# Kernel tuning notes

Hardware: AMD Instinct MI355X
Metric: run time of the kernel (lower is better)

The kernel has to match this reference:

```python
import jax, jax.numpy as jnp
import numpy as np

B, T, INP, E, H, N = 16, 256, 1536, 512, 8, 16
D = E // H            # 64, must equal default dim_head for to_out shapes to work
SCALE = D ** -0.5
EPS = 1e-5


def _ln(x, g, b):
    m = x.mean(-1, keepdims=True)
    v = ((x - m) ** 2).mean(-1, keepdims=True)
    return (x - m) * jax.lax.rsqrt(v + EPS) * g + b


def _attend(q, k, v, Wo, bo):
    # q,k,v: [bt, h, n, d]. NOTE: attend is LogSoftmax, not Softmax (faithful).
    dots = jnp.einsum('bhnd,bhmd->bhnm', q, k) * SCALE
    a = jax.nn.log_softmax(dots, axis=-1)
    o = jnp.einsum('bhnm,bhmd->bhnd', a, v)
    o = o.transpose(0, 2, 1, 3).reshape(o.shape[0], N, E)  # b n (h d)
    return o @ Wo + bo


def _self_attn(x, Wqkv, Wo, bo):
    # x is already LayerNormed (PreNorm); residual adds the normed x (faithful).
    qkv = x @ Wqkv  # [bt, n, 3E]
    q, k, v = jnp.split(qkv, 3, axis=-1)
    hd = lambda t: t.reshape(t.shape[0], N, H, D).transpose(0, 2, 1, 3)
    return _attend(hd(q), hd(k), hd(v), Wo, bo) + x


def _ff(x, W1, b1, W2, b2):
    # x already LayerNormed; residual adds normed x (faithful to PreNorm+FF).
    return jax.nn.gelu(x @ W1 + b1, approximate=False) @ W2 + b2 + x


def setup_inputs() -> dict:
    key = jax.random.key(0)
    ks = iter(jax.random.split(key, 64))
    nrm = lambda shape, s=0.02: jax.random.normal(next(ks), shape, jnp.float32) * s
    inp = {
        'features': jax.random.normal(next(ks), (B, T, INP), jnp.float32),
        'targets_array': jax.random.randint(next(ks), (B, T), 0, N, jnp.int64),
        'emb': nrm((N, E), 1.0),
        'Wf': nrm((INP, 2 * E * N)), 'bf': jnp.zeros((2 * E * N,), jnp.float32),
        # layer 0: Attention (tuple path: only to_out used)
        'att0_Wo': nrm((E, E)), 'att0_bo': jnp.zeros((E,), jnp.float32),
        'Wm': nrm((E, 1)), 'bm': jnp.zeros((1,), jnp.float32),
    }
    for i in range(3):
        inp[f'ff{i}_g'] = jnp.ones((E,), jnp.float32)
        inp[f'ff{i}_b'] = jnp.zeros((E,), jnp.float32)
        inp[f'ff{i}_W1'] = nrm((E, 2 * E)); inp[f'ff{i}_b1'] = jnp.zeros((2 * E,), jnp.float32)
        inp[f'ff{i}_W2'] = nrm((2 * E, E)); inp[f'ff{i}_b2'] = jnp.zeros((E,), jnp.float32)
    for i in (1, 2):
        inp[f'att{i}_g'] = jnp.ones((E,), jnp.float32)
        inp[f'att{i}_b'] = jnp.zeros((E,), jnp.float32)
        inp[f'att{i}_Wqkv'] = nrm((E, 3 * E))
        inp[f'att{i}_Wo'] = nrm((E, E)); inp[f'att{i}_bo'] = jnp.zeros((E,), jnp.float32)
    return inp


def reference(features, targets_array, emb, Wf, bf, att0_Wo, att0_bo, Wm, bm,
              ff0_g, ff0_b, ff0_W1, ff0_b1, ff0_W2, ff0_b2,
              ff1_g, ff1_b, ff1_W1, ff1_b1, ff1_W2, ff1_b2,
              ff2_g, ff2_b, ff2_W1, ff2_b1, ff2_W2, ff2_b2,
              att1_g, att1_b, att1_Wqkv, att1_Wo, att1_bo,
              att2_g, att2_b, att2_Wqkv, att2_Wo, att2_bo):
    f = features.reshape(-1, INP)                 # [BT, INP]
    t = targets_array.reshape(-1)                 # [BT]
    kv = f @ Wf + bf                              # [BT, 2*E*N]
    k_, v_ = jnp.split(kv, 2, axis=-1)
    nhd = lambda x: x.reshape(-1, N, H, D).transpose(0, 2, 1, 3)  # b (n h d) -> b h n d
    k, v = nhd(k_), nhd(v_)
    q = emb[t].reshape(-1, H, 1, D)               # b h d -> b h 1 d
    q = jnp.broadcast_to(q, (q.shape[0], H, N, D))
    # layer stack: Attn(tuple), PreNorm(FF), PreNorm(Attn), PreNorm(FF), PreNorm(Attn), PreNorm(FF)
    x = _attend(q, k, v, att0_Wo, att0_bo)        # [BT, N, E]
    x = _ff(_ln(x, ff0_g, ff0_b), ff0_W1, ff0_b1, ff0_W2, ff0_b2)
    x = _self_attn(_ln(x, att1_g, att1_b), att1_Wqkv, att1_Wo, att1_bo)
    x = _ff(_ln(x, ff1_g, ff1_b), ff1_W1, ff1_b1, ff1_W2, ff1_b2)
    x = _self_attn(_ln(x, att2_g, att2_b), att2_Wqkv, att2_Wo, att2_bo)
    x = _ff(_ln(x, ff2_g, ff2_b), ff2_W1, ff2_b1, ff2_W2, ff2_b2)
    out = x.mean(axis=1)                          # mean over targets -> [BT, E]
    out = out.reshape(B, T, E)
    mean = out @ Wm + bm                          # [B, T, 1]
    return mean
```

## Files before the change

kernel.cpp:

```cpp
#include <hip/hip_runtime.h>
#include <math.h>

#define BTOT 4096
#define INP  1536
#define EDIM 512
#define NTOK 16
#define KVW  16384
#define ENW  8192
#define FFH  1024
#define NDOT 2048

typedef __attribute__((ext_vector_type(8))) __bf16 bf16x8;
typedef __attribute__((ext_vector_type(4))) float f32x4;

__device__ __forceinline__ ushort f2bf(float f) {
    union { float f; unsigned u; } v; v.f = f;
    unsigned r = v.u + 0x7fffu + ((v.u >> 16) & 1u);
    return (ushort)(r >> 16);
}
__device__ __forceinline__ float bf2f(ushort h) {
    union { unsigned u; float f; } v; v.u = ((unsigned)h) << 16;
    return v.f;
}

__device__ __forceinline__ void transpose_body(
    const float* in, int ld, int c0, int R, ushort* out,
    int bx, int by, int tid)
{
    __shared__ float t[64][65];
    const int bc = bx * 64 + c0;
    const int br = by * 64;
#pragma unroll
    for (int it = 0; it < 16; ++it) {
        int idx = tid + it * 256;
        int r = idx >> 6, c = idx & 63;
        t[r][c] = in[(size_t)(br + r) * ld + bc + c];
    }
    __syncthreads();
    const int C0 = bx * 64;
#pragma unroll
    for (int it = 0; it < 4; ++it) {
        int idx = tid + it * 256;
        int cc = idx >> 4, rp = idx & 15;
        uint2 w2;
        w2.x = f2bf(t[4 * rp + 0][cc]) | ((unsigned)f2bf(t[4 * rp + 1][cc]) << 16);
        w2.y = f2bf(t[4 * rp + 2][cc]) | ((unsigned)f2bf(t[4 * rp + 3][cc]) << 16);
        *reinterpret_cast<uint2*>(out + (size_t)(C0 + cc) * R + br + 4 * rp) = w2;
    }
}

struct TJob { const float* in; ushort* out; int ld, c0, R, gbx, gby, boffs; };
struct TJobs { TJob j[10]; };

__global__ __launch_bounds__(256) void transpose_all_k(TJobs jobs)
{
    const int b = blockIdx.x;
    int ji = 0;
    while (ji < 9 && b >= jobs.j[ji + 1].boffs) ++ji;
    TJob jb = jobs.j[ji];
    const int rel = b - jb.boffs;
    transpose_body(jb.in, jb.ld, jb.c0, jb.R, jb.out,
                   rel % jb.gbx, rel / jb.gbx, threadIdx.x);
}

__global__ __launch_bounds__(256) void conv_all_k(
    const float* __restrict__ features, ushort* __restrict__ featb,
    const float* __restrict__ wq0, const float* __restrict__ wq1,
    ushort* __restrict__ wv0, ushort* __restrict__ wv1)
{
    const int b = blockIdx.x;
    if (b < 3072) {
        const int i = b * 256 + threadIdx.x;
        const float4* p = reinterpret_cast<const float4*>(features) + 2 * (size_t)i;
        float4 a = p[0], c = p[1];
        uint4 o;
        o.x = f2bf(a.x) | ((unsigned)f2bf(a.y) << 16);
        o.y = f2bf(a.z) | ((unsigned)f2bf(a.w) << 16);
        o.z = f2bf(c.x) | ((unsigned)f2bf(c.y) << 16);
        o.w = f2bf(c.z) | ((unsigned)f2bf(c.w) << 16);
        reinterpret_cast<uint4*>(featb)[i] = o;
    } else {
        const int bb = b - 3072;
        const float* src = (bb >= 128) ? wq1 : wq0;
        ushort* dst = (bb >= 128) ? wv1 : wv0;
        const int idx = (bb & 127) * 256 + threadIdx.x;
        const int row = idx >> 6, c8 = (idx & 63) * 8;
        const float4* p = reinterpret_cast<const float4*>(
            src + (size_t)row * (3 * EDIM) + 2 * EDIM + c8);
        float4 a = p[0], c = p[1];
        uint4 o;
        o.x = f2bf(a.x) | ((unsigned)f2bf(a.y) << 16);
        o.y = f2bf(a.z) | ((unsigned)f2bf(a.w) << 16);
        o.z = f2bf(c.x) | ((unsigned)f2bf(c.y) << 16);
        o.w = f2bf(c.z) | ((unsigned)f2bf(c.w) << 16);
        *reinterpret_cast<uint4*>(dst + (size_t)row * EDIM + c8) = o;
    }
}

__global__ __launch_bounds__(256) void gproj_k(
    const float* __restrict__ Wf, const float* __restrict__ bfv,
    const float* __restrict__ emb, ushort* __restrict__ BTg,
    float* __restrict__ C0s, const int* __restrict__ targets,
    int* __restrict__ perm, int* __restrict__ boff)
{
    if (blockIdx.y == 8) {
        if (blockIdx.x != 0) return;
        __shared__ int cnt[NTOK], off_s[NTOK], cur[NTOK];
        const int tid = threadIdx.x;
        if (tid < NTOK) cnt[tid] = 0;
        __syncthreads();
        for (int i = tid; i < BTOT; i += 256) atomicAdd(&cnt[targets[i]], 1);
        __syncthreads();
        if (tid == 0) {
            int s = 0;
            for (int b = 0; b < NTOK; ++b) { off_s[b] = s; cur[b] = s; s += cnt[b]; }
            for (int b = 0; b < NTOK; ++b) boff[b] = off_s[b];
            boff[NTOK] = s;
        }
        __syncthreads();
        for (int i = tid; i < BTOT; i += 256) {
            int t = targets[i];
            int p = atomicAdd(&cur[t], 1);
            perm[p] = i;
        }
        return;
    }

    const int hm = blockIdx.x;
    const int h = hm >> 4, m = hm & 15;
    const int l = threadIdx.x & 63, w = threadIdx.x >> 6;
    const int t = l & 15, isub = l >> 4;
    const int colb = m * 512 + h * 64;
    const int ibase = blockIdx.y * (INP / 8);

    float4 e[16];
#pragma unroll
    for (int q = 0; q < 16; ++q)
        e[q] = *reinterpret_cast<const float4*>(emb + t * EDIM + h * 64 + q * 4);

    const int n = t * 128 + hm;
    for (int i0 = ibase; i0 < ibase + INP / 8; i0 += 16) {
        const int i = i0 + w * 4 + isub;
        const float* wr = Wf + (size_t)i * KVW + colb;
        float acc = 0.f;
#pragma unroll
        for (int q = 0; q < 16; ++q) {
            float4 v4 = *reinterpret_cast<const float4*>(wr + q * 4);
            acc = fmaf(v4.x, e[q].x, fmaf(v4.y, e[q].y,
                  fmaf(v4.z, e[q].z, fmaf(v4.w, e[q].w, acc))));
        }
        BTg[(size_t)n * INP + i] = f2bf(acc);
    }
    if (blockIdx.y == 0 && w == 0 && isub == 0) {
        const float* br = bfv + colb;
        float acc = 0.f;
#pragma unroll
        for (int q = 0; q < 16; ++q) {
            float4 v4 = *reinterpret_cast<const float4*>(br + q * 4);
            acc = fmaf(v4.x, e[q].x, fmaf(v4.y, e[q].y,
                  fmaf(v4.z, e[q].z, fmaf(v4.w, e[q].w, acc))));
        }
        C0s[n] = 0.125f * acc;
    }
}

template <int BM, int BN, int WM, int WN, int NW, bool GELU, bool OUTBF>
__global__ __launch_bounds__(NW * 64) void gemm_mfma_k(
    const ushort* __restrict__ A, int lda,
    const ushort* __restrict__ BT, int ldb,
    void* __restrict__ Cp, int ldc, int K,
    const float* __restrict__ bias,
    const float* __restrict__ res, int ldr,
    float scale)
{
    static_assert((BM / WM) * (BN / WN) == NW, "wave grid");
    static_assert(BM % (NW * 8) == 0 && BN % (NW * 8) == 0, "staging");
    constexpr int FM = WM / 16, FN = WN / 16;
    constexpr int IA = BM * 8 / (NW * 64), IB = BN * 8 / (NW * 64);
    constexpr int RA = BM / NW, RB = BN / NW;

    __shared__ bf16x8 As[BM][8];
    __shared__ bf16x8 Bs[BN][8];
    const int tid = threadIdx.x;
    const int l   = tid & 63;
    const int w   = tid >> 6;
    const int wm  = w / (BN / WN), wn = w % (BN / WN);
    const int brow = blockIdx.y * BM, bcol = blockIdx.x * BN;

    const int lr = l >> 3;
    const int ls = (l & 7) ^ lr;
    const ushort* Ab = A  + (size_t)(brow + w * RA + lr) * lda + ls * 8;
    const ushort* Bb = BT + (size_t)(bcol + w * RB + lr) * ldb + ls * 8;

    f32x4 acc[FM][FN];
#pragma unroll
    for (int i = 0; i < FM; ++i)
#pragma unroll
        for (int j = 0; j < FN; ++j) acc[i][j] = (f32x4)0.f;

    for (int k0 = 0; k0 < K; k0 += 64) {
#pragma unroll
        for (int i = 0; i < IA; ++i)
            __builtin_amdgcn_global_load_lds(
                (const __attribute__((address_space(1))) void*)(Ab + (size_t)(i * 8) * lda + k0),
                (__attribute__((address_space(3))) void*)&As[w * RA + i * 8][0],
                16, 0, 0);
#pragma unroll
        for (int i = 0; i < IB; ++i)
            __builtin_amdgcn_global_load_lds(
                (const __attribute__((address_space(1))) void*)(Bb + (size_t)(i * 8) * ldb + k0),
                (__attribute__((address_space(3))) void*)&Bs[w * RB + i * 8][0],
                16, 0, 0);
        __syncthreads();
#pragma unroll
        for (int kh = 0; kh < 2; ++kh) {
            const int slot = (kh * 4 + (l >> 4)) ^ (l & 7);
            bf16x8 af[FM], bfr[FN];
#pragma unroll
            for (int mt = 0; mt < FM; ++mt)
                af[mt] = As[wm * WM + mt * 16 + (l & 15)][slot];
#pragma unroll
            for (int nt = 0; nt < FN; ++nt)
                bfr[nt] = Bs[wn * WN + nt * 16 + (l & 15)][slot];
#pragma unroll
            for (int mt = 0; mt < FM; ++mt)
#pragma unroll
                for (int nt = 0; nt < FN; ++nt)
                    acc[mt][nt] = __builtin_amdgcn_mfma_f32_16x16x32_bf16(
                        af[mt], bfr[nt], acc[mt][nt], 0, 0, 0);
        }
        __syncthreads();
    }

    const int cr = (l >> 4) * 4, cc = l & 15;
#pragma unroll
    for (int mt = 0; mt < FM; ++mt) {
#pragma unroll
        for (int nt = 0; nt < FN; ++nt) {
            const int gc = bcol + wn * WN + nt * 16 + cc;
            const float bv = bias ? bias[gc] : 0.f;
#pragma unroll
            for (int r = 0; r < 4; ++r) {
                const size_t gr = (size_t)brow + wm * WM + mt * 16 + cr + r;
                float v = acc[mt][nt][r] * scale + bv;
                if (GELU) v = 0.5f * v * (1.f + erff(v * 0.70710678118654752f));
                if (res) v += res[gr * ldr + gc];
                if (OUTBF) ((ushort*)Cp)[gr * ldc + gc] = f2bf(v);
                else       ((float*)Cp)[gr * ldc + gc]  = v;
            }
        }
    }
}

__global__ __launch_bounds__(256) void gemm_dots_k(
    const ushort* __restrict__ A,
    const ushort* __restrict__ BT,
    const int* __restrict__ perm, const int* __restrict__ boff,
    const float* __restrict__ C0s, float* __restrict__ Csel)
{
    const int bucket = blockIdx.y;
    const int off = boff[bucket], end = boff[bucket + 1];
    const int tile = blockIdx.x;
    if (tile * 128 >= end - off) return;

    __shared__ bf16x8 As[128][8];
    __shared__ bf16x8 Bs[128][8];
    const int tid = threadIdx.x;
    const int l = tid & 63, w = tid >> 6;
    const int wm = w >> 1, wn = w & 1;
    const int lr = l >> 3;
    const int ls = (l & 7) ^ lr;

    int rowidx[4];
#pragma unroll
    for (int i = 0; i < 4; ++i) {
        int rg = off + tile * 128 + w * 32 + lr + i * 8;
        rowidx[i] = perm[rg < end ? rg : off];
    }
    const ushort* Bb = BT + (size_t)(bucket * 128 + w * 32 + lr) * INP + ls * 8;

    f32x4 acc[4][4];
#pragma unroll
    for (int i = 0; i < 4; ++i)
#pragma unroll
        for (int j = 0; j < 4; ++j) acc[i][j] = (f32x4)0.f;

    for (int k0 = 0; k0 < INP; k0 += 64) {
#pragma unroll
        for (int i = 0; i < 4; ++i)
            __builtin_amdgcn_global_load_lds(
                (const __attribute__((address_space(1))) void*)(
                    A + (size_t)rowidx[i] * INP + ls * 8 + k0),
                (__attribute__((address_space(3))) void*)&As[w * 32 + i * 8][0],
                16, 0, 0);
#pragma unroll
        for (int i = 0; i < 4; ++i)
            __builtin_amdgcn_global_load_lds(
                (const __attribute__((address_space(1))) void*)(
                    Bb + (size_t)(i * 8) * INP + k0),
                (__attribute__((address_space(3))) void*)&Bs[w * 32 + i * 8][0],
                16, 0, 0);
        __syncthreads();
#pragma unroll
        for (int kh = 0; kh < 2; ++kh) {
            const int slot = (kh * 4 + (l >> 4)) ^ (l & 7);
            bf16x8 af[4], bfr[4];
#pragma unroll
            for (int mt = 0; mt < 4; ++mt)
                af[mt] = As[wm * 64 + mt * 16 + (l & 15)][slot];
#pragma unroll
            for (int nt = 0; nt < 4; ++nt)
                bfr[nt] = Bs[wn * 64 + nt * 16 + (l & 15)][slot];
#pragma unroll
            for (int mt = 0; mt < 4; ++mt)
#pragma unroll
                for (int nt = 0; nt < 4; ++nt)
                    acc[mt][nt] = __builtin_amdgcn_mfma_f32_16x16x32_bf16(
                        af[mt], bfr[nt], acc[mt][nt], 0, 0, 0);
        }
        __syncthreads();
    }

    const int cr = (l >> 4) * 4, cc = l & 15;
#pragma unroll
    for (int mt = 0; mt < 4; ++mt) {
#pragma unroll
        for (int nt = 0; nt < 4; ++nt) {
            const int gc = wn * 64 + nt * 16 + cc;
            const float bv = C0s[bucket * 128 + gc];
#pragma unroll
            for (int r = 0; r < 4; ++r) {
                float val = acc[mt][nt][r] * 0.125f + bv;
                float mx = val;
                mx = fmaxf(mx, __shfl_xor(mx, 1, 64));
                mx = fmaxf(mx, __shfl_xor(mx, 2, 64));
                mx = fmaxf(mx, __shfl_xor(mx, 4, 64));
                mx = fmaxf(mx, __shfl_xor(mx, 8, 64));
                float e = expf(val - mx);
                e += __shfl_xor(e, 1, 64);
                e += __shfl_xor(e, 2, 64);
                e += __shfl_xor(e, 4, 64);
                e += __shfl_xor(e, 8, 64);
                const float lse = mx + logf(e);
                int rg = off + tile * 128 + wm * 64 + mt * 16 + cr + r;
                int orow = perm[rg < end ? rg : off];
                Csel[(size_t)orow * 128 + gc] = val - lse;
            }
        }
    }
}

__global__ __launch_bounds__(512) void attend0_k(
    const float* __restrict__ dsel, const ushort* __restrict__ vb,
    ushort* __restrict__ o)
{
    const int bt = blockIdx.x;
    const int l  = threadIdx.x & 63;
    const int h  = threadIdx.x >> 6;
    const int dg = l & 7, mg = l >> 3;

    const float w0 = dsel[(size_t)bt * 128 + h * 16 + mg];
    const float w1 = dsel[(size_t)bt * 128 + h * 16 + 8 + mg];

    const ushort* base = vb + (size_t)bt * ENW + h * 64 + dg * 8;
    uint4 v0 = *reinterpret_cast<const uint4*>(base + (size_t)mg * EDIM);
    uint4 v1 = *reinterpret_cast<const uint4*>(base + (size_t)(8 + mg) * EDIM);
    const ushort* u0 = reinterpret_cast<const ushort*>(&v0);
    const ushort* u1 = reinterpret_cast<const ushort*>(&v1);
    float acc[8];
#pragma unroll
    for (int j = 0; j < 8; ++j)
        acc[j] = w0 * bf2f(u0[j]) + w1 * bf2f(u1[j]);
#pragma unroll
    for (int off = 8; off < 64; off <<= 1)
#pragma unroll
        for (int j = 0; j < 8; ++j) acc[j] += __shfl_xor(acc[j], off, 64);

    if (mg == 0) {
        uint4 pk;
        pk.x = f2bf(acc[0]) | ((unsigned)f2bf(acc[1]) << 16);
        pk.y = f2bf(acc[2]) | ((unsigned)f2bf(acc[3]) << 16);
        pk.z = f2bf(acc[4]) | ((unsigned)f2bf(acc[5]) << 16);
        pk.w = f2bf(acc[6]) | ((unsigned)f2bf(acc[7]) << 16);
        *reinterpret_cast<uint4*>(o + (size_t)bt * EDIM + h * 64 + dg * 8) = pk;
    }
}

__global__ __launch_bounds__(256) void ln_k(
    const float* __restrict__ x, const float* __restrict__ g,
    const float* __restrict__ b, float* __restrict__ y,
    ushort* __restrict__ yb)
{
    const int row = blockIdx.x * 4 + (threadIdx.x >> 6);
    const int lane = threadIdx.x & 63;
    const float* xr = x + (size_t)row * EDIM + lane * 8;
    float4 a0 = *reinterpret_cast<const float4*>(xr);
    float4 a1 = *reinterpret_cast<const float4*>(xr + 4);
    float v[8] = {a0.x, a0.y, a0.z, a0.w, a1.x, a1.y, a1.z, a1.w};

    float s = 0.f;
#pragma unroll
    for (int j = 0; j < 8; ++j) s += v[j];
#pragma unroll
    for (int off = 32; off; off >>= 1) s += __shfl_xor(s, off, 64);
    const float m = s * (1.f / 512.f);

    float q = 0.f;
#pragma unroll
    for (int j = 0; j < 8; ++j) { float d = v[j] - m; q = fmaf(d, d, q); }
#pragma unroll
    for (int off = 32; off; off >>= 1) q += __shfl_xor(q, off, 64);
    const float inv = rsqrtf(q * (1.f / 512.f) + 1e-5f);

    const int c = lane * 8;
    float4 g0 = *reinterpret_cast<const float4*>(g + c);
    float4 g1 = *reinterpret_cast<const float4*>(g + c + 4);
    float4 b0 = *reinterpret_cast<const float4*>(b + c);
    float4 b1 = *reinterpret_cast<const float4*>(b + c + 4);
    float gg[8] = {g0.x, g0.y, g0.z, g0.w, g1.x, g1.y, g1.z, g1.w};
    float bb[8] = {b0.x, b0.y, b0.z, b0.w, b1.x, b1.y, b1.z, b1.w};
    float out[8];
#pragma unroll
    for (int j = 0; j < 8; ++j) out[j] = (v[j] - m) * inv * gg[j] + bb[j];
    float* yr = y + (size_t)row * EDIM + c;
    *reinterpret_cast<float4*>(yr) = make_float4(out[0], out[1], out[2], out[3]);
    *reinterpret_cast<float4*>(yr + 4) = make_float4(out[4], out[5], out[6], out[7]);
    uint4 p;
    p.x = f2bf(out[0]) | ((unsigned)f2bf(out[1]) << 16);
    p.y = f2bf(out[2]) | ((unsigned)f2bf(out[3]) << 16);
    p.z = f2bf(out[4]) | ((unsigned)f2bf(out[5]) << 16);
    p.w = f2bf(out[6]) | ((unsigned)f2bf(out[7]) << 16);
    *reinterpret_cast<uint4*>(yb + (size_t)row * EDIM + c) = p;
}

__global__ __launch_bounds__(256) void final_k(
    const float* __restrict__ x, const float* __restrict__ Wm,
    const float* __restrict__ bm, float* __restrict__ out)
{
    const int row = blockIdx.x * 4 + (threadIdx.x >> 6);
    const int lane = threadIdx.x & 63;
    const float* xr = x + (size_t)row * EDIM + lane * 8;
    const float* wr = Wm + lane * 8;
    float s = 0.f;
#pragma unroll
    for (int j = 0; j < 8; ++j) s = fmaf(xr[j], wr[j], s);
#pragma unroll
    for (int off = 32; off; off >>= 1) s += __shfl_xor(s, off, 64);
    if (lane == 0) out[row] = s + bm[0];
}

extern "C" void kernel_launch(void* const* d_in, const int* in_sizes, int n_in,
                              void* d_out, int out_size, void* d_ws, size_t ws_size,
                              hipStream_t stream)
{
    (void)in_sizes; (void)n_in; (void)out_size;
    const float* features = (const float*)d_in[0];
    const int*   targets  = (const int*)d_in[1];
    const float* emb      = (const float*)d_in[2];
    const float* Wf       = (const float*)d_in[3];
    const float* bfv      = (const float*)d_in[4];
    const float* a0Wo     = (const float*)d_in[5];
    const float* a0bo     = (const float*)d_in[6];
    const float* Wm       = (const float*)d_in[7];
    const float* bm       = (const float*)d_in[8];
    const float *ffg[3], *ffb[3], *W1[3], *b1[3], *W2[3], *b2[3];
    for (int i = 0; i < 3; ++i) {
        ffg[i] = (const float*)d_in[9 + 6 * i];
        ffb[i] = (const float*)d_in[10 + 6 * i];
        W1[i]  = (const float*)d_in[11 + 6 * i];
        b1[i]  = (const float*)d_in[12 + 6 * i];
        W2[i]  = (const float*)d_in[13 + 6 * i];
        b2[i]  = (const float*)d_in[14 + 6 * i];
    }
    const float *ag[2], *abp[2], *aWqkv[2], *aWo[2], *abo[2];
    for (int i = 0; i < 2; ++i) {
        ag[i]    = (const float*)d_in[27 + 5 * i];
        abp[i]   = (const float*)d_in[28 + 5 * i];
        aWqkv[i] = (const float*)d_in[29 + 5 * i];
        aWo[i]   = (const float*)d_in[30 + 5 * i];
        abo[i]   = (const float*)d_in[31 + 5 * i];
    }

    char* wsc = (char*)d_ws;
    auto alloc = [&](size_t bytes) { char* p = wsc; wsc += bytes; return p; };
    ushort* WfvT  = (ushort*)alloc((size_t)ENW * INP * 2);
    ushort* BTg   = (ushort*)alloc((size_t)NDOT * INP * 2);
    float*  C0s   = (float*) alloc((size_t)NDOT * 4);
    float*  dsel  = (float*) alloc((size_t)BTOT * 128 * 4);
    int*    perm  = (int*)   alloc((size_t)BTOT * 4);
    int*    boff  = (int*)   alloc(32 * 4);
    ushort* a0WoT = (ushort*)alloc((size_t)EDIM * EDIM * 2);
    ushort *W1T[3], *W2T[3], *WoT[2], *Wv_bf[2], *WcombT[2];
    for (int i = 0; i < 3; ++i) {
        W1T[i] = (ushort*)alloc((size_t)FFH * EDIM * 2);
        W2T[i] = (ushort*)alloc((size_t)EDIM * FFH * 2);
    }
    for (int i = 0; i < 2; ++i) {
        WoT[i]    = (ushort*)alloc((size_t)EDIM * EDIM * 2);
        Wv_bf[i]  = (ushort*)alloc((size_t)EDIM * EDIM * 2);
        WcombT[i] = (ushort*)alloc((size_t)EDIM * EDIM * 2);
    }
    ushort* featb = (ushort*)alloc((size_t)BTOT * INP * 2);
    ushort* o_b   = (ushort*)alloc((size_t)BTOT * EDIM * 2);
    float*  x     = (float*) alloc((size_t)BTOT * EDIM * 4);
    float*  xln   = (float*) alloc((size_t)BTOT * EDIM * 4);
    ushort* xlnb  = (ushort*)alloc((size_t)BTOT * EDIM * 2);
    ushort* hb    = (ushort*)alloc((size_t)BTOT * FFH * 2);
    const size_t fixed = (size_t)(wsc - (char*)d_ws);
    int CB = BTOT;
    while (CB > 256 && fixed + (size_t)CB * ENW * 2 > ws_size) CB >>= 1;
    ushort* vb = (ushort*)alloc((size_t)CB * ENW * 2);

    const dim3 blk(256, 1, 1);

    conv_all_k<<<3328, blk, 0, stream>>>(features, featb,
                                         aWqkv[0], aWqkv[1], Wv_bf[0], Wv_bf[1]);
    gproj_k<<<dim3(128, 9), blk, 0, stream>>>(Wf, bfv, emb, BTg, C0s,
                                              targets, perm, boff);

    TJobs tj;
    int ob = 0, ji = 0;
    auto addj = [&](const float* in, ushort* out, int ld, int c0, int R,
                    int gbx, int gby) {
        tj.j[ji++] = {in, out, ld, c0, R, gbx, gby, ob};
        ob += gbx * gby;
    };
    addj(Wf, WfvT, KVW, ENW, INP, 128, 24);
    addj(a0Wo, a0WoT, EDIM, 0, EDIM, 8, 8);
    for (int i = 0; i < 3; ++i) {
        addj(W1[i], W1T[i], FFH, 0, EDIM, 16, 8);
        addj(W2[i], W2T[i], EDIM, 0, FFH, 8, 16);
    }
    addj(aWo[0], WoT[0], EDIM, 0, EDIM, 8, 8);
    addj(aWo[1], WoT[1], EDIM, 0, EDIM, 8, 8);
    transpose_all_k<<<ob, blk, 0, stream>>>(tj);

    const float CATT = -44.36141955583650f;
    for (int i = 0; i < 2; ++i)
        gemm_mfma_k<64, 128, 32, 64, 4, false, true>
            <<<dim3(EDIM / 128, EDIM / 64), blk, 0, stream>>>(
            WoT[i], EDIM, Wv_bf[i], EDIM, WcombT[i], EDIM, EDIM,
            nullptr, nullptr, 0, CATT);

    gemm_dots_k<<<dim3(32, 16), blk, 0, stream>>>(featb, BTg, perm, boff,
                                                  C0s, dsel);
    for (int c0 = 0; c0 < BTOT; c0 += CB) {
        gemm_mfma_k<128, 128, 64, 64, 4, false, true>
            <<<dim3(ENW / 128, CB / 128), blk, 0, stream>>>(
            featb + (size_t)c0 * INP, INP, WfvT, INP, vb, ENW, INP,
            bfv + ENW, nullptr, 0, 1.f);
        attend0_k<<<CB, 512, 0, stream>>>(dsel + (size_t)c0 * 128, vb,
                                          o_b + (size_t)c0 * EDIM);
    }
    gemm_mfma_k<64, 128, 32, 64, 4, false, false>
        <<<dim3(EDIM / 128, BTOT / 64), blk, 0, stream>>>(
        o_b, EDIM, a0WoT, EDIM, x, EDIM, EDIM, a0bo, nullptr, 0, 1.f);

    auto ln = [&](const float* g, const float* b) {
        ln_k<<<BTOT / 4, blk, 0, stream>>>(x, g, b, xln, xlnb);
    };
    auto ff = [&](int i) {
        ln(ffg[i], ffb[i]);
        gemm_mfma_k<64, 128, 32, 64, 4, true, true>
            <<<dim3(FFH / 128, BTOT / 64), blk, 0, stream>>>(
            xlnb, EDIM, W1T[i], EDIM, hb, FFH, EDIM, b1[i], nullptr, 0, 1.f);
        gemm_mfma_k<64, 128, 32, 64, 4, false, false>
            <<<dim3(EDIM / 128, BTOT / 64), blk, 0, stream>>>(
            hb, FFH, W2T[i], FFH, x, EDIM, FFH, b2[i], xln, EDIM, 1.f);
    };
    auto attn = [&](int i) {
        ln(ag[i], abp[i]);
        gemm_mfma_k<64, 128, 32, 64, 4, false, false>
            <<<dim3(EDIM / 128, BTOT / 64), blk, 0, stream>>>(
            xlnb, EDIM, WcombT[i], EDIM, x, EDIM, EDIM, abo[i], xln, EDIM, 1.f);
    };

    ff(0);
    attn(0);
    ff(1);
    attn(1);
    ff(2);

    final_k<<<BTOT / 4, blk, 0, stream>>>(x, Wm, bm, (float*)d_out);
}
```

Measured before the change: 492.6 us.

## Merge prep kernels and independent GEMMs into single heterogeneous launches

Folds the bf16 conversion, the gproj/bucketing and the weight-transpose kernels into one prep launch. It also merges the big V projection GEMM, the bucketed dots GEMM and the two small Wo·Wv combine GEMMs into one multi-job GEMM launch that dispatches on block index. This removes several kernel launches and lets the independent GEMMs fill the GPU together. The cost is dropping the workspace-size chunking, so the whole V buffer (4096x8192 bf16) must fit in workspace, and the prep kernel now carries extra shared memory for every block.

Result: no change. 493.5 us (+0.2%).

```diff
diff --git a/kernel.cpp b/kernel.cpp
--- a/kernel.cpp
+++ b/kernel.cpp
@@ -23,18 +23,129 @@
     return v.f;
 }
 
-__device__ __forceinline__ void transpose_body(
-    const float* in, int ld, int c0, int R, ushort* out,
-    int bx, int by, int tid)
+struct TJob { const float* in; ushort* out; int ld, c0, R, gbx, boffs; };
+
+struct PrepArgs {
+    const float* features; ushort* featb;
+    const float* wq0; const float* wq1; ushort* wv0; ushort* wv1;
+    const float* Wf; const float* bfv; const float* emb;
+    ushort* BTg; float* C0s; const int* targets; int* perm; int* boff;
+    TJob tj[10];
+};
+
+__global__ __launch_bounds__(256) void prep_all_k(PrepArgs A)
 {
     __shared__ float t[64][65];
-    const int bc = bx * 64 + c0;
+    __shared__ int cnt[NTOK], off_s[NTOK], cur[NTOK];
+    const int b = blockIdx.x;
+    const int tid = threadIdx.x;
+
+    if (b < 3328) {
+        if (b < 3072) {
+            const int i = b * 256 + tid;
+            const float4* p = reinterpret_cast<const float4*>(A.features) + 2 * (size_t)i;
+            float4 a = p[0], c = p[1];
+            uint4 o;
+            o.x = f2bf(a.x) | ((unsigned)f2bf(a.y) << 16);
+            o.y = f2bf(a.z) | ((unsigned)f2bf(a.w) << 16);
+            o.z = f2bf(c.x) | ((unsigned)f2bf(c.y) << 16);
+            o.w = f2bf(c.z) | ((unsigned)f2bf(c.w) << 16);
+            reinterpret_cast<uint4*>(A.featb)[i] = o;
+        } else {
+            const int bb = b - 3072;
+            const float* src = (bb >= 128) ? A.wq1 : A.wq0;
+            ushort* dst = (bb >= 128) ? A.wv1 : A.wv0;
+            const int idx = (bb & 127) * 256 + tid;
+            const int row = idx >> 6, c8 = (idx & 63) * 8;
+            const float4* p = reinterpret_cast<const float4*>(
+                src + (size_t)row * (3 * EDIM) + 2 * EDIM + c8);
+            float4 a = p[0], c = p[1];
+            uint4 o;
+            o.x = f2bf(a.x) | ((unsigned)f2bf(a.y) << 16);
+            o.y = f2bf(a.z) | ((unsigned)f2bf(a.w) << 16);
+            o.z = f2bf(c.x) | ((unsigned)f2bf(c.y) << 16);
+            o.w = f2bf(c.z) | ((unsigned)f2bf(c.w) << 16);
+            *reinterpret_cast<uint4*>(dst + (size_t)row * EDIM + c8) = o;
+        }
+        return;
+    }
+
+    if (b < 4480) {
+        const int gb = b - 3328;
+        const int hm = gb & 127;
+        const int gby = gb >> 7;
+        if (gby == 8) {
+            if (hm != 0) return;
+            if (tid < NTOK) cnt[tid] = 0;
+            __syncthreads();
+            for (int i = tid; i < BTOT; i += 256) atomicAdd(&cnt[A.targets[i]], 1);
+            __syncthreads();
+            if (tid == 0) {
+                int s = 0;
+                for (int bk = 0; bk < NTOK; ++bk) { off_s[bk] = s; cur[bk] = s; s += cnt[bk]; }
+                for (int bk = 0; bk < NTOK; ++bk) A.boff[bk] = off_s[bk];
+                A.boff[NTOK] = s;
+            }
+            __syncthreads();
+            for (int i = tid; i < BTOT; i += 256) {
+                int tt = A.targets[i];
+                int p = atomicAdd(&cur[tt], 1);
+                A.perm[p] = i;
+            }
+            return;
+        }
+        const int h = hm >> 4, m = hm & 15;
+        const int l = tid & 63, w = tid >> 6;
+        const int tk = l & 15, isub = l >> 4;
+        const int colb = m * 512 + h * 64;
+        const int ibase = gby * (INP / 8);
+
+        float4 e[16];
+#pragma unroll
+        for (int q = 0; q < 16; ++q)
+            e[q] = *reinterpret_cast<const float4*>(A.emb + tk * EDIM + h * 64 + q * 4);
+
+        const int n = tk * 128 + hm;
+        for (int i0 = ibase; i0 < ibase + INP / 8; i0 += 16) {
+            const int i = i0 + w * 4 + isub;
+            const float* wr = A.Wf + (size_t)i * KVW + colb;
+            float acc = 0.f;
+#pragma unroll
+            for (int q = 0; q < 16; ++q) {
+                float4 v4 = *reinterpret_cast<const float4*>(wr + q * 4);
+                acc = fmaf(v4.x, e[q].x, fmaf(v4.y, e[q].y,
+                      fmaf(v4.z, e[q].z, fmaf(v4.w, e[q].w, acc))));
+            }
+            A.BTg[(size_t)n * INP + i] = f2bf(acc);
+        }
+        if (gby == 0 && w == 0 && isub == 0) {
+            const float* br = A.bfv + colb;
+            float acc = 0.f;
+#pragma unroll
+            for (int q = 0; q < 16; ++q) {
+                float4 v4 = *reinterpret_cast<const float4*>(br + q * 4);
+                acc = fmaf(v4.x, e[q].x, fmaf(v4.y, e[q].y,
+                      fmaf(v4.z, e[q].z, fmaf(v4.w, e[q].w, acc))));
+            }
+            A.C0s[n] = 0.125f * acc;
+        }
+        return;
+    }
+
+    const int rel = b - 4480;
+    int ji = 0;
+    while (ji < 9 && rel >= A.tj[ji + 1].boffs) ++ji;
+    TJob jb = A.tj[ji];
+    const int r2 = rel - jb.boffs;
+    const int bx = r2 % jb.gbx, by = r2 / jb.gbx;
+
+    const int bc = bx * 64 + jb.c0;
     const int br = by * 64;
 #pragma unroll
     for (int it = 0; it < 16; ++it) {
         int idx = tid + it * 256;
         int r = idx >> 6, c = idx & 63;
-        t[r][c] = in[(size_t)(br + r) * ld + bc + c];
+        t[r][c] = jb.in[(size_t)(br + r) * jb.ld + bc + c];
     }
     __syncthreads();
     const int C0 = bx * 64;
@@ -45,122 +156,7 @@
         uint2 w2;
         w2.x = f2bf(t[4 * rp + 0][cc]) | ((unsigned)f2bf(t[4 * rp + 1][cc]) << 16);
         w2.y = f2bf(t[4 * rp + 2][cc]) | ((unsigned)f2bf(t[4 * rp + 3][cc]) << 16);
-        *reinterpret_cast<uint2*>(out + (size_t)(C0 + cc) * R + br + 4 * rp) = w2;
-    }
-}
-
-struct TJob { const float* in; ushort* out; int ld, c0, R, gbx, gby, boffs; };
-struct TJobs { TJob j[10]; };
-
-__global__ __launch_bounds__(256) void transpose_all_k(TJobs jobs)
-{
-    const int b = blockIdx.x;
-    int ji = 0;
-    while (ji < 9 && b >= jobs.j[ji + 1].boffs) ++ji;
-    TJob jb = jobs.j[ji];
-    const int rel = b - jb.boffs;
-    transpose_body(jb.in, jb.ld, jb.c0, jb.R, jb.out,
-                   rel % jb.gbx, rel / jb.gbx, threadIdx.x);
-}
-
-__global__ __launch_bounds__(256) void conv_all_k(
-    const float* __restrict__ features, ushort* __restrict__ featb,
-    const float* __restrict__ wq0, const float* __restrict__ wq1,
-    ushort* __restrict__ wv0, ushort* __restrict__ wv1)
-{
-    const int b = blockIdx.x;
-    if (b < 3072) {
-        const int i = b * 256 + threadIdx.x;
-        const float4* p = reinterpret_cast<const float4*>(features) + 2 * (size_t)i;
-        float4 a = p[0], c = p[1];
-        uint4 o;
-        o.x = f2bf(a.x) | ((unsigned)f2bf(a.y) << 16);
-        o.y = f2bf(a.z) | ((unsigned)f2bf(a.w) << 16);
-        o.z = f2bf(c.x) | ((unsigned)f2bf(c.y) << 16);
-        o.w = f2bf(c.z) | ((unsigned)f2bf(c.w) << 16);
-        reinterpret_cast<uint4*>(featb)[i] = o;
-    } else {
-        const int bb = b - 3072;
-        const float* src = (bb >= 128) ? wq1 : wq0;
-        ushort* dst = (bb >= 128) ? wv1 : wv0;
-        const int idx = (bb & 127) * 256 + threadIdx.x;
-        const int row = idx >> 6, c8 = (idx & 63) * 8;
-        const float4* p = reinterpret_cast<const float4*>(
-            src + (size_t)row * (3 * EDIM) + 2 * EDIM + c8);
-        float4 a = p[0], c = p[1];
-        uint4 o;
-        o.x = f2bf(a.x) | ((unsigned)f2bf(a.y) << 16);
-        o.y = f2bf(a.z) | ((unsigned)f2bf(a.w) << 16);
-        o.z = f2bf(c.x) | ((unsigned)f2bf(c.y) << 16);
-        o.w = f2bf(c.z) | ((unsigned)f2bf(c.w) << 16);
-        *reinterpret_cast<uint4*>(dst + (size_t)row * EDIM + c8) = o;
-    }
-}
-
-__global__ __launch_bounds__(256) void gproj_k(
-    const float* __restrict__ Wf, const float* __restrict__ bfv,
-    const float* __restrict__ emb, ushort* __restrict__ BTg,
-    float* __restrict__ C0s, const int* __restrict__ targets,
-    int* __restrict__ perm, int* __restrict__ boff)
-{
-    if (blockIdx.y == 8) {
-        if (blockIdx.x != 0) return;
-        __shared__ int cnt[NTOK], off_s[NTOK], cur[NTOK];
-        const int tid = threadIdx.x;
-        if (tid < NTOK) cnt[tid] = 0;
-        __syncthreads();
-        for (int i = tid; i < BTOT; i += 256) atomicAdd(&cnt[targets[i]], 1);
-        __syncthreads();
-        if (tid == 0) {
-            int s = 0;
-            for (int b = 0; b < NTOK; ++b) { off_s[b] = s; cur[b] = s; s += cnt[b]; }
-            for (int b = 0; b < NTOK; ++b) boff[b] = off_s[b];
-            boff[NTOK] = s;
-        }
-        __syncthreads();
-        for (int i = tid; i < BTOT; i += 256) {
-            int t = targets[i];
-            int p = atomicAdd(&cur[t], 1);
-            perm[p] = i;
-        }
-        return;
-    }
-
-    const int hm = blockIdx.x;
-    const int h = hm >> 4, m = hm & 15;
-    const int l = threadIdx.x & 63, w = threadIdx.x >> 6;
-    const int t = l & 15, isub = l >> 4;
-    const int colb = m * 512 + h * 64;
-    const int ibase = blockIdx.y * (INP / 8);
-
-    float4 e[16];
-#pragma unroll
-    for (int q = 0; q < 16; ++q)
-        e[q] = *reinterpret_cast<const float4*>(emb + t * EDIM + h * 64 + q * 4);
-
-    const int n = t * 128 + hm;
-    for (int i0 = ibase; i0 < ibase + INP / 8; i0 += 16) {
-        const int i = i0 + w * 4 + isub;
-        const float* wr = Wf + (size_t)i * KVW + colb;
-        float acc = 0.f;
-#pragma unroll
-        for (int q = 0; q < 16; ++q) {
-            float4 v4 = *reinterpret_cast<const float4*>(wr + q * 4);
-            acc = fmaf(v4.x, e[q].x, fmaf(v4.y, e[q].y,
-                  fmaf(v4.z, e[q].z, fmaf(v4.w, e[q].w, acc))));
-        }
-        BTg[(size_t)n * INP + i] = f2bf(acc);
-    }
-    if (blockIdx.y == 0 && w == 0 && isub == 0) {
-        const float* br = bfv + colb;
-        float acc = 0.f;
-#pragma unroll
-        for (int q = 0; q < 16; ++q) {
-            float4 v4 = *reinterpret_cast<const float4*>(br + q * 4);
-            acc = fmaf(v4.x, e[q].x, fmaf(v4.y, e[q].y,
-                  fmaf(v4.z, e[q].z, fmaf(v4.w, e[q].w, acc))));
-        }
-        C0s[n] = 0.125f * acc;
+        *reinterpret_cast<uint2*>(jb.out + (size_t)(C0 + cc) * jb.R + br + 4 * rp) = w2;
     }
 }
 
@@ -252,32 +248,64 @@
     }
 }
 
-__global__ __launch_bounds__(256) void gemm_dots_k(
-    const ushort* __restrict__ A,
-    const ushort* __restrict__ BT,
+__global__ __launch_bounds__(256) void mega_gemm_k(
+    const ushort* __restrict__ featb,
+    const ushort* __restrict__ WfvT, const float* __restrict__ bfvv,
+    ushort* __restrict__ vb,
+    const ushort* __restrict__ BTg,
     const int* __restrict__ perm, const int* __restrict__ boff,
-    const float* __restrict__ C0s, float* __restrict__ Csel)
+    const float* __restrict__ C0s, float* __restrict__ dsel,
+    const ushort* __restrict__ WoT0, const ushort* __restrict__ Wv0,
+    ushort* __restrict__ WC0,
+    const ushort* __restrict__ WoT1, const ushort* __restrict__ Wv1,
+    ushort* __restrict__ WC1)
 {
-    const int bucket = blockIdx.y;
-    const int off = boff[bucket], end = boff[bucket + 1];
-    const int tile = blockIdx.x;
-    if (tile * 128 >= end - off) return;
-
     __shared__ bf16x8 As[128][8];
     __shared__ bf16x8 Bs[128][8];
+    const int b = blockIdx.x;
     const int tid = threadIdx.x;
     const int l = tid & 63, w = tid >> 6;
     const int wm = w >> 1, wn = w & 1;
-    const int lr = l >> 3;
-    const int ls = (l & 7) ^ lr;
-
-    int rowidx[4];
-#pragma unroll
-    for (int i = 0; i < 4; ++i) {
-        int rg = off + tile * 128 + w * 32 + lr + i * 8;
-        rowidx[i] = perm[rg < end ? rg : off];
-    }
-    const ushort* Bb = BT + (size_t)(bucket * 128 + w * 32 + lr) * INP + ls * 8;
+    const int lr = l >> 3, ls = (l & 7) ^ lr;
+
+    int jtype, K;
+    const ushort* Asrc[4];
+    const ushort* Bb;
+    ushort* WCo = nullptr;
+    int brow = 0, bcol = 0, bucket = 0, off = 0, end = 0, tile = 0;
+
+    if (b < 2048) {
+        jtype = 0; K = INP;
+        brow = (b >> 6) * 128; bcol = (b & 63) * 128;
+#pragma unroll
+        for (int i = 0; i < 4; ++i)
+            Asrc[i] = featb + (size_t)(brow + w * 32 + lr + i * 8) * INP + ls * 8;
+        Bb = WfvT + (size_t)(bcol + w * 32 + lr) * INP + ls * 8;
+    } else if (b < 2560) {
+        jtype = 1; K = INP;
+        const int rel = b - 2048;
+        bucket = rel >> 5; tile = rel & 31;
+        off = boff[bucket]; end = boff[bucket + 1];
+        if (tile * 128 >= end - off) return;
+#pragma unroll
+        for (int i = 0; i < 4; ++i) {
+            int rg = off + tile * 128 + w * 32 + lr + i * 8;
+            Asrc[i] = featb + (size_t)perm[rg < end ? rg : off] * INP + ls * 8;
+        }
+        Bb = BTg + (size_t)(bucket * 128 + w * 32 + lr) * INP + ls * 8;
+    } else {
+        jtype = 2; K = EDIM;
+        const int rel = b - 2560;
+        const int wi = rel >> 4, r2 = rel & 15;
+        brow = (r2 >> 2) * 128; bcol = (r2 & 3) * 128;
+        const ushort* Ai = wi ? WoT1 : WoT0;
+        const ushort* Bi = wi ? Wv1 : Wv0;
+        WCo = wi ? WC1 : WC0;
+#pragma unroll
+        for (int i = 0; i < 4; ++i)
+            Asrc[i] = Ai + (size_t)(brow + w * 32 + lr + i * 8) * EDIM + ls * 8;
+        Bb = Bi + (size_t)(bcol + w * 32 + lr) * EDIM + ls * 8;
+    }
 
     f32x4 acc[4][4];
 #pragma unroll
@@ -285,19 +313,17 @@
 #pragma unroll
         for (int j = 0; j < 4; ++j) acc[i][j] = (f32x4)0.f;
 
-    for (int k0 = 0; k0 < INP; k0 += 64) {
+    for (int k0 = 0; k0 < K; k0 += 64) {
 #pragma unroll
         for (int i = 0; i < 4; ++i)
             __builtin_amdgcn_global_load_lds(
-                (const __attribute__((address_space(1))) void*)(
-                    A + (size_t)rowidx[i] * INP + ls * 8 + k0),
+                (const __attribute__((address_space(1))) void*)(Asrc[i] + k0),
                 (__attribute__((address_space(3))) void*)&As[w * 32 + i * 8][0],
                 16, 0, 0);
 #pragma unroll
         for (int i = 0; i < 4; ++i)
             __builtin_amdgcn_global_load_lds(
-                (const __attribute__((address_space(1))) void*)(
-                    Bb + (size_t)(i * 8) * INP + k0),
+                (const __attribute__((address_space(1))) void*)(Bb + (size_t)(i * 8) * K + k0),
                 (__attribute__((address_space(3))) void*)&Bs[w * 32 + i * 8][0],
                 16, 0, 0);
         __syncthreads();
@@ -322,29 +348,60 @@
     }
 
     const int cr = (l >> 4) * 4, cc = l & 15;
-#pragma unroll
-    for (int mt = 0; mt < 4; ++mt) {
-#pragma unroll
-        for (int nt = 0; nt < 4; ++nt) {
-            const int gc = wn * 64 + nt * 16 + cc;
-            const float bv = C0s[bucket * 128 + gc];
-#pragma unroll
-            for (int r = 0; r < 4; ++r) {
-                float val = acc[mt][nt][r] * 0.125f + bv;
-                float mx = val;
-                mx = fmaxf(mx, __shfl_xor(mx, 1, 64));
-                mx = fmaxf(mx, __shfl_xor(mx, 2, 64));
-                mx = fmaxf(mx, __shfl_xor(mx, 4, 64));
-                mx = fmaxf(mx, __shfl_xor(mx, 8, 64));
-                float e = expf(val - mx);
-                e += __shfl_xor(e, 1, 64);
-                e += __shfl_xor(e, 2, 64);
-                e += __shfl_xor(e, 4, 64);
-                e += __shfl_xor(e, 8, 64);
-                const float lse = mx + logf(e);
-                int rg = off + tile * 128 + wm * 64 + mt * 16 + cr + r;
-                int orow = perm[rg < end ? rg : off];
-                Csel[(size_t)orow * 128 + gc] = val - lse;
+    const float CATT = -44.36141955583650f;
+
+    if (jtype == 0) {
+#pragma unroll
+        for (int mt = 0; mt < 4; ++mt) {
+#pragma unroll
+            for (int nt = 0; nt < 4; ++nt) {
+                const int gc = bcol + wn * 64 + nt * 16 + cc;
+                const float bv = bfvv[gc];
+#pragma unroll
+                for (int r = 0; r < 4; ++r) {
+                    const size_t gr = (size_t)brow + wm * 64 + mt * 16 + cr + r;
+                    vb[gr * ENW + gc] = f2bf(acc[mt][nt][r] + bv);
+                }
+            }
+        }
+    } else if (jtype == 1) {
+#pragma unroll
+        for (int mt = 0; mt < 4; ++mt) {
+#pragma unroll
+            for (int nt = 0; nt < 4; ++nt) {
+                const int gc = wn * 64 + nt * 16 + cc;
+                const float bv = C0s[bucket * 128 + gc];
+#pragma unroll
+                for (int r = 0; r < 4; ++r) {
+                    float val = acc[mt][nt][r] * 0.125f + bv;
+                    float mx = val;
+                    mx = fmaxf(mx, __shfl_xor(mx, 1, 64));
+                    mx = fmaxf(mx, __shfl_xor(mx, 2, 64));
+                    mx = fmaxf(mx, __shfl_xor(mx, 4, 64));
+                    mx = fmaxf(mx, __shfl_xor(mx, 8, 64));
+                    float e = expf(val - mx);
+                    e += __shfl_xor(e, 1, 64);
+                    e += __shfl_xor(e, 2, 64);
+                    e += __shfl_xor(e, 4, 64);
+                    e += __shfl_xor(e, 8, 64);
+                    const float lse = mx + logf(e);
+                    int rg = off + tile * 128 + wm * 64 + mt * 16 + cr + r;
+                    int orow = perm[rg < end ? rg : off];
+                    dsel[(size_t)orow * 128 + gc] = val - lse;
+                }
+            }
+        }
+    } else {
+#pragma unroll
+        for (int mt = 0; mt < 4; ++mt) {
+#pragma unroll
+            for (int nt = 0; nt < 4; ++nt) {
+                const int gc = bcol + wn * 64 + nt * 16 + cc;
+#pragma unroll
+                for (int r = 0; r < 4; ++r) {
+                    const size_t gr = (size_t)brow + wm * 64 + mt * 16 + cr + r;
+                    WCo[gr * EDIM + gc] = f2bf(acc[mt][nt][r] * CATT);
+                }
             }
         }
     }
@@ -453,7 +510,7 @@
                               void* d_out, int out_size, void* d_ws, size_t ws_size,
                               hipStream_t stream)
 {
-    (void)in_sizes; (void)n_in; (void)out_size;
+    (void)in_sizes; (void)n_in; (void)out_size; (void)ws_size;
     const float* features = (const float*)d_in[0];
     const int*   targets  = (const int*)d_in[1];
     const float* emb      = (const float*)d_in[2];
@@ -506,23 +563,20 @@
     float*  xln   = (float*) alloc((size_t)BTOT * EDIM * 4);
     ushort* xlnb  = (ushort*)alloc((size_t)BTOT * EDIM * 2);
     ushort* hb    = (ushort*)alloc((size_t)BTOT * FFH * 2);
-    const size_t fixed = (size_t)(wsc - (char*)d_ws);
-    int CB = BTOT;
-    while (CB > 256 && fixed + (size_t)CB * ENW * 2 > ws_size) CB >>= 1;
-    ushort* vb = (ushort*)alloc((size_t)CB * ENW * 2);
+    ushort* vb    = (ushort*)alloc((size_t)BTOT * ENW * 2);
 
     const dim3 blk(256, 1, 1);
 
-    conv_all_k<<<3328, blk, 0, stream>>>(features, featb,
-                                         aWqkv[0], aWqkv[1], Wv_bf[0], Wv_bf[1]);
-    gproj_k<<<dim3(128, 9), blk, 0, stream>>>(Wf, bfv, emb, BTg, C0s,
-                                              targets, perm, boff);
-
-    TJobs tj;
+    PrepArgs pa;
+    pa.features = features; pa.featb = featb;
+    pa.wq0 = aWqkv[0]; pa.wq1 = aWqkv[1]; pa.wv0 = Wv_bf[0]; pa.wv1 = Wv_bf[1];
+    pa.Wf = Wf; pa.bfv = bfv; pa.emb = emb;
+    pa.BTg = BTg; pa.C0s = C0s; pa.targets = targets;
+    pa.perm = perm; pa.boff = boff;
     int ob = 0, ji = 0;
     auto addj = [&](const float* in, ushort* out, int ld, int c0, int R,
                     int gbx, int gby) {
-        tj.j[ji++] = {in, out, ld, c0, R, gbx, gby, ob};
+        pa.tj[ji++] = {in, out, ld, c0, R, gbx, ob};
         ob += gbx * gby;
     };
     addj(Wf, WfvT, KVW, ENW, INP, 128, 24);
@@ -533,25 +587,15 @@
     }
     addj(aWo[0], WoT[0], EDIM, 0, EDIM, 8, 8);
     addj(aWo[1], WoT[1], EDIM, 0, EDIM, 8, 8);
-    transpose_all_k<<<ob, blk, 0, stream>>>(tj);
-
-    const float CATT = -44.36141955583650f;
-    for (int i = 0; i < 2; ++i)
-        gemm_mfma_k<64, 128, 32, 64, 4, false, true>
-            <<<dim3(EDIM / 128, EDIM / 64), blk, 0, stream>>>(
-            WoT[i], EDIM, Wv_bf[i], EDIM, WcombT[i], EDIM, EDIM,
-            nullptr, nullptr, 0, CATT);
-
-    gemm_dots_k<<<dim3(32, 16), blk, 0, stream>>>(featb, BTg, perm, boff,
-                                                  C0s, dsel);
-    for (int c0 = 0; c0 < BTOT; c0 += CB) {
-        gemm_mfma_k<128, 128, 64, 64, 4, false, true>
-            <<<dim3(ENW / 128, CB / 128), blk, 0, stream>>>(
-            featb + (size_t)c0 * INP, INP, WfvT, INP, vb, ENW, INP,
-            bfv + ENW, nullptr, 0, 1.f);
-        attend0_k<<<CB, 512, 0, stream>>>(dsel + (size_t)c0 * 128, vb,
-                                          o_b + (size_t)c0 * EDIM);
-    }
+    prep_all_k<<<4480 + ob, blk, 0, stream>>>(pa);
+
+    mega_gemm_k<<<2592, blk, 0, stream>>>(
+        featb, WfvT, bfv + ENW, vb,
+        BTg, perm, boff, C0s, dsel,
+        WoT[0], Wv_bf[0], WcombT[0],
+        WoT[1], Wv_bf[1], WcombT[1]);
+
+    attend0_k<<<BTOT, 512, 0, stream>>>(dsel, vb, o_b);
     gemm_mfma_k<64, 128, 32, 64, 4, false, false>
         <<<dim3(EDIM / 128, BTOT / 64), blk, 0, stream>>>(
         o_b, EDIM, a0WoT, EDIM, x, EDIM, EDIM, a0bo, nullptr, 0, 1.f);
```

## Add 256x256 double-buffered direct-to-LDS GEMM for the value projection

Applied to the files above, without the earlier changes.

Replaces the generic 128x128 MFMA GEMM for the large features x Wf value projection with a dedicated 256x256-tile kernel of 512 threads. It double-buffers global-to-LDS loads with XOR-swizzled slots and interleaves the next tile's prefetch with the MFMA phases, using barriers and setprio. The workspace chunking loop is removed so the whole value buffer is allocated at once and attend0 runs in a single launch. This assumes the workspace is large enough for the full bf16 value buffer and drops the fallback for smaller workspaces.

After: 474.0 us. -3.8%, faster.

```diff
diff --git a/kernel.cpp b/kernel.cpp
--- a/kernel.cpp
+++ b/kernel.cpp
@@ -49,7 +49,7 @@
     }
 }
 
-struct TJob { const float* in; ushort* out; int ld, c0, R, gbx, gby, boffs; };
+struct TJob { const float* in; ushort* out; int ld, c0, R, gbx, boffs; };
 struct TJobs { TJob j[10]; };
 
 __global__ __launch_bounds__(256) void transpose_all_k(TJobs jobs)
@@ -252,6 +252,117 @@
     }
 }
 
+__global__ __launch_bounds__(512, 2) void gemm_v256_k(
+    const ushort* __restrict__ A,
+    const ushort* __restrict__ BT,
+    const float* __restrict__ bias,
+    ushort* __restrict__ C)
+{
+    __shared__ bf16x8 lds[2][2][256][8];
+    const int tid = threadIdx.x;
+    const int l = tid & 63, w = tid >> 6;
+    const int wm = w >> 2, wn = w & 3;
+    const int brow = blockIdx.y * 256, bcol = blockIdx.x * 256;
+    const int lr = l >> 3, ls = (l & 7) ^ lr;
+
+    const ushort* Ab = A  + (size_t)(brow + w * 8 + lr) * INP + ls * 8;
+    const ushort* Bb = BT + (size_t)(bcol + w * 8 + lr) * INP + ls * 8;
+
+#define STAGE_T(d, t) do { const int k0s = (t) * 64;                          \
+    _Pragma("unroll")                                                          \
+    for (int g = 0; g < 4; ++g)                                                \
+        __builtin_amdgcn_global_load_lds(                                      \
+            (const __attribute__((address_space(1))) void*)(Ab + (size_t)(g * 64) * INP + k0s), \
+            (__attribute__((address_space(3))) void*)&lds[d][0][g * 64 + w * 8][0], 16, 0, 0);  \
+    _Pragma("unroll")                                                          \
+    for (int g = 0; g < 4; ++g)                                                \
+        __builtin_amdgcn_global_load_lds(                                      \
+            (const __attribute__((address_space(1))) void*)(Bb + (size_t)(g * 64) * INP + k0s), \
+            (__attribute__((address_space(3))) void*)&lds[d][1][g * 64 + w * 8][0], 16, 0, 0);  \
+} while (0)
+
+    f32x4 acc[8][4];
+#pragma unroll
+    for (int i = 0; i < 8; ++i)
+#pragma unroll
+        for (int j = 0; j < 4; ++j) acc[i][j] = (f32x4)0.f;
+
+    STAGE_T(0, 0);
+    STAGE_T(1, 1);
+    asm volatile("s_waitcnt vmcnt(8)" ::: "memory");
+    __builtin_amdgcn_s_barrier();
+
+    const int NT = INP / 64;
+    for (int j = 0; j < NT; ++j) {
+        const int d = j & 1;
+        const bool st = (j > 0 && j < NT - 1);
+        const int k0s = (j + 1) * 64;
+        bf16x8 bfr[4][2];
+#pragma unroll
+        for (int p = 0; p < 4; ++p) {
+            const int rh = p >> 1, kh = p & 1;
+            const int slot = (kh * 4 + (l >> 4)) ^ (l & 7);
+            bf16x8 a[4];
+#pragma unroll
+            for (int mt = 0; mt < 4; ++mt)
+                a[mt] = lds[d][0][wm * 128 + rh * 64 + mt * 16 + (l & 15)][slot];
+            if (p < 2) {
+#pragma unroll
+                for (int nt = 0; nt < 4; ++nt)
+                    bfr[nt][kh] = lds[d][1][wn * 64 + nt * 16 + (l & 15)][slot];
+            }
+            if (st) {
+#pragma unroll
+                for (int q = 0; q < 2; ++q) {
+                    const int idx = 2 * p + q;
+                    if (idx < 4)
+                        __builtin_amdgcn_global_load_lds(
+                            (const __attribute__((address_space(1))) void*)(
+                                Ab + (size_t)(idx * 64) * INP + k0s),
+                            (__attribute__((address_space(3))) void*)
+                                &lds[d ^ 1][0][idx * 64 + w * 8][0], 16, 0, 0);
+                    else
+                        __builtin_amdgcn_global_load_lds(
+                            (const __attribute__((address_space(1))) void*)(
+                                Bb + (size_t)((idx - 4) * 64) * INP + k0s),
+                            (__attribute__((address_space(3))) void*)
+                                &lds[d ^ 1][1][(idx - 4) * 64 + w * 8][0], 16, 0, 0);
+                }
+            }
+            __builtin_amdgcn_s_barrier();
+            asm volatile("s_waitcnt lgkmcnt(0)" ::: "memory");
+            __builtin_amdgcn_sched_barrier(0);
+            __builtin_amdgcn_s_setprio(1);
+#pragma unroll
+            for (int mt = 0; mt < 4; ++mt)
+#pragma unroll
+                for (int nt = 0; nt < 4; ++nt)
+                    acc[rh * 4 + mt][nt] = __builtin_amdgcn_mfma_f32_16x16x32_bf16(
+                        a[mt], bfr[nt][kh], acc[rh * 4 + mt][nt], 0, 0, 0);
+            __builtin_amdgcn_s_setprio(0);
+            if (p == 3) asm volatile("s_waitcnt vmcnt(0)" ::: "memory");
+            __builtin_amdgcn_s_barrier();
+        }
+    }
+#undef STAGE_T
+
+    const int cr = (l >> 4) * 4, cc = l & 15;
+#pragma unroll
+    for (int h = 0; h < 2; ++h)
+#pragma unroll
+        for (int mt = 0; mt < 4; ++mt)
+#pragma unroll
+            for (int nt = 0; nt < 4; ++nt) {
+                const int gc = bcol + wn * 64 + nt * 16 + cc;
+                const float bv = bias[gc];
+#pragma unroll
+                for (int r = 0; r < 4; ++r) {
+                    const size_t gr = (size_t)brow + wm * 128 + h * 64 + mt * 16 + cr + r;
+                    C[gr * ENW + gc] = f2bf(acc[h * 4 + mt][nt][r] + bv);
+                }
+            }
+}
+
 __global__ __launch_bounds__(256) void gemm_dots_k(
     const ushort* __restrict__ A,
     const ushort* __restrict__ BT,
@@ -453,7 +564,7 @@
                               void* d_out, int out_size, void* d_ws, size_t ws_size,
                               hipStream_t stream)
 {
-    (void)in_sizes; (void)n_in; (void)out_size;
+    (void)in_sizes; (void)n_in; (void)out_size; (void)ws_size;
     const float* features = (const float*)d_in[0];
     const int*   targets  = (const int*)d_in[1];
     const float* emb      = (const float*)d_in[2];
@@ -506,10 +617,7 @@
     float*  xln   = (float*) alloc((size_t)BTOT * EDIM * 4);
     ushort* xlnb  = (ushort*)alloc((size_t)BTOT * EDIM * 2);
     ushort* hb    = (ushort*)alloc((size_t)BTOT * FFH * 2);
-    const size_t fixed = (size_t)(wsc - (char*)d_ws);
-    int CB = BTOT;
-    while (CB > 256 && fixed + (size_t)CB * ENW * 2 > ws_size) CB >>= 1;
-    ushort* vb = (ushort*)alloc((size_t)CB * ENW * 2);
+    ushort* vb    = (ushort*)alloc((size_t)BTOT * ENW * 2);
 
     const dim3 blk(256, 1, 1);
 
@@ -522,7 +630,7 @@
     int ob = 0, ji = 0;
     auto addj = [&](const float* in, ushort* out, int ld, int c0, int R,
                     int gbx, int gby) {
-        tj.j[ji++] = {in, out, ld, c0, R, gbx, gby, ob};
+        tj.j[ji++] = {in, out, ld, c0, R, gbx, ob};
         ob += gbx * gby;
     };
     addj(Wf, WfvT, KVW, ENW, INP, 128, 24);
@@ -536,22 +644,16 @@
     transpose_all_k<<<ob, blk, 0, stream>>>(tj);
 
     const float CATT = -44.36141955583650f;
+    gemm_dots_k<<<dim3(32, 16), blk, 0, stream>>>(featb, BTg, perm, boff,
+                                                  C0s, dsel);
     for (int i = 0; i < 2; ++i)
         gemm_mfma_k<64, 128, 32, 64, 4, false, true>
             <<<dim3(EDIM / 128, EDIM / 64), blk, 0, stream>>>(
             WoT[i], EDIM, Wv_bf[i], EDIM, WcombT[i], EDIM, EDIM,
             nullptr, nullptr, 0, CATT);
-
-    gemm_dots_k<<<dim3(32, 16), blk, 0, stream>>>(featb, BTg, perm, boff,
-                                                  C0s, dsel);
-    for (int c0 = 0; c0 < BTOT; c0 += CB) {
-        gemm_mfma_k<128, 128, 64, 64, 4, false, true>
-            <<<dim3(ENW / 128, CB / 128), blk, 0, stream>>>(
-            featb + (size_t)c0 * INP, INP, WfvT, INP, vb, ENW, INP,
-            bfv + ENW, nullptr, 0, 1.f);
-        attend0_k<<<CB, 512, 0, stream>>>(dsel + (size_t)c0 * 128, vb,
-                                          o_b + (size_t)c0 * EDIM);
-    }
+    gemm_v256_k<<<dim3(ENW / 256, BTOT / 256), dim3(512, 1, 1), 0, stream>>>(
+        featb, WfvT, bfv + ENW, vb);
+    attend0_k<<<BTOT, 512, 0, stream>>>(dsel, vb, o_b);
     gemm_mfma_k<64, 128, 32, 64, 4, false, false>
         <<<dim3(EDIM / 128, BTOT / 64), blk, 0, stream>>>(
         o_b, EDIM, a0WoT, EDIM, x, EDIM, EDIM, a0bo, nullptr, 0, 1.f);
```
